# Kernel tuning notes

Measured on AMD Instinct MI355X. Metric: run time of the kernel, lower is better.

The kernel has to match this reference:

```python
import jax, jax.numpy as jnp
import numpy as np

# Pyramid of RBS (Givens) gates on 6 wires: 15 gates, column-major diamond order.
PYRAMID_PAIRS = [(0,1),(1,2),(0,1),(2,3),(1,2),(3,4),(0,1),(2,3),(4,5),(1,2),(3,4),(0,1),(2,3),(1,2),(0,1)]


def setup_inputs() -> dict:
    key = jax.random.key(0)
    k1, k2, k3, k4, k5, k6 = jax.random.split(key, 6)
    B = 65536
    return {
        "inputs": jax.random.normal(k1, (B, 28, 28), dtype=jnp.float32),
        "dense_w": jax.random.normal(k2, (784, 6), dtype=jnp.float32) * 0.05,
        "dense_b": jax.random.normal(k3, (6,), dtype=jnp.float32) * 0.05,
        # module initializes quantum_weights to zeros; use small random angles for a
        # non-degenerate reference (zeros makes the pyramid the identity)
        "qweights": jax.random.normal(k4, (15,), dtype=jnp.float32) * 0.1,
        "out_w": jax.random.normal(k5, (6, 1), dtype=jnp.float32) * 0.5,
        "out_b": jax.random.normal(k6, (1,), dtype=jnp.float32) * 0.1,
    }


def _quantum_block(h, qweights):
    # vector_loader: encode normalized h into unary amplitudes (Hamming-weight-1 subspace)
    a = h / jnp.linalg.norm(h, axis=1, keepdims=True)  # [B, 6]; NaN if zero norm, sanitized below
    # pyramid_circuit: each RBS(theta) acts as a 2x2 Givens rotation on unary amplitudes
    for k, (i, j) in enumerate(PYRAMID_PAIRS):
        c, s = jnp.cos(qweights[k]), jnp.sin(qweights[k])
        ai, aj = a[:, i], a[:, j]
        a = a.at[:, i].set(c * ai + s * aj)
        a = a.at[:, j].set(-s * ai + c * aj)
    # <Z_i> on a unary state = 1 - 2 * P(qubit i = 1) = 1 - 2 * a_i^2
    z = 1.0 - 2.0 * a * a
    return jnp.where(jnp.isnan(z), jnp.zeros_like(z), z)


def reference(inputs, dense_w, dense_b, qweights, out_w, out_b):
    x = inputs.reshape(inputs.shape[0], -1)          # flatten [B, 784]
    h = x @ dense_w + dense_b                        # Dense(6, linear)
    z = _quantum_block(h, qweights)                  # batched statevector sim, [B, 6]
    return jax.nn.sigmoid(z @ out_w + out_b)         # Dense(1, sigmoid)
```

## Files before the change

kernel.cpp:

```cpp
#include <hip/hip_runtime.h>
#include <math.h>

#define TPB 256

__global__ __launch_bounds__(TPB) void hybrid_kernel(
    const float* __restrict__ inp,
    const float* __restrict__ dw,
    const float* __restrict__ db,
    const float* __restrict__ qw,
    const float* __restrict__ ow,
    const float* __restrict__ ob,
    float* __restrict__ out,
    int B)
{
    __shared__ float4 wT4[6 * 196];
    __shared__ float csc[15], css[15];
    __shared__ float sb[8], sw[8];
    __shared__ float sob;

    float* wT = (float*)wT4;
    const int tid = threadIdx.x;

    for (int i = tid; i < 4704; i += TPB) {
        int e = i / 6;
        int j = i - e * 6;
        wT[j * 784 + e] = dw[i];
    }
    if (tid < 15) { float q = qw[tid]; csc[tid] = cosf(q); css[tid] = sinf(q); }
    if (tid < 6)  { sb[tid] = db[tid]; sw[tid] = ow[tid]; }
    if (tid == 0) sob = ob[0];
    __syncthreads();

    const int lane = tid & 63;
    const int grp  = lane >> 4;
    const int gl   = lane & 15;
    const int row  = blockIdx.x * 16 + (tid >> 6) * 4 + grp;
    if (row >= B) return;

    const float4* x4 = (const float4*)(inp + (size_t)row * 784);

    float acc[6] = {0.f, 0.f, 0.f, 0.f, 0.f, 0.f};

    #pragma unroll 4
    for (int t = 0; t < 12; ++t) {
        const int idx4 = gl + 16 * t;
        const float4 xv = x4[idx4];
        #pragma unroll
        for (int j = 0; j < 6; ++j) {
            const float4 wv = wT4[j * 196 + idx4];
            acc[j] += xv.x * wv.x + xv.y * wv.y + xv.z * wv.z + xv.w * wv.w;
        }
    }
    if (gl < 4) {
        const int idx4 = 192 + gl;
        const float4 xv = x4[idx4];
        #pragma unroll
        for (int j = 0; j < 6; ++j) {
            const float4 wv = wT4[j * 196 + idx4];
            acc[j] += xv.x * wv.x + xv.y * wv.y + xv.z * wv.z + xv.w * wv.w;
        }
    }

    #pragma unroll
    for (int m = 1; m <= 8; m <<= 1) {
        #pragma unroll
        for (int j = 0; j < 6; ++j)
            acc[j] += __shfl_xor(acc[j], m, 64);
    }

    float a[6];
    float hh = 0.f;
    #pragma unroll
    for (int j = 0; j < 6; ++j) {
        a[j] = acc[j] + sb[j];
        hh += a[j] * a[j];
    }
    const float inv = rsqrtf(hh);
    #pragma unroll
    for (int j = 0; j < 6; ++j) a[j] *= inv;

    const int PI[15] = {0,1,0,2,1,3,0,2,4,1,3,0,2,1,0};
    #pragma unroll
    for (int k = 0; k < 15; ++k) {
        const int i = PI[k];
        const float c = csc[k], s = css[k];
        const float ai = a[i], aj = a[i + 1];
        a[i]     = c * ai + s * aj;
        a[i + 1] = c * aj - s * ai;
    }

    float v = sob;
    #pragma unroll
    for (int j = 0; j < 6; ++j) {
        float z = 1.f - 2.f * a[j] * a[j];
        z = isnan(z) ? 0.f : z;
        v += z * sw[j];
    }
    const float o = 1.f / (1.f + __expf(-v));

    if (gl == 0) out[row] = o;
}

extern "C" void kernel_launch(void* const* d_in, const int* in_sizes, int n_in,
                              void* d_out, int out_size, void* d_ws, size_t ws_size,
                              hipStream_t stream) {
    const float* inp = (const float*)d_in[0];
    const float* dw  = (const float*)d_in[1];
    const float* db  = (const float*)d_in[2];
    const float* qw  = (const float*)d_in[3];
    const float* ow  = (const float*)d_in[4];
    const float* ob  = (const float*)d_in[5];
    float* out = (float*)d_out;

    const int B = in_sizes[0] / 784;
    const int blocks = (B + 15) / 16;
    hybrid_kernel<<<blocks, TPB, 0, stream>>>(inp, dw, db, qw, ow, ob, out, B);
}
```

Before: 292.8 us.

## Map one row per thread with register double-buffered input loads

Switches from 16 lanes cooperating per row to one thread per row, streaming the row through two register buffers of float4 chunks so the next chunk's load overlaps the current chunk's dot products. Drops the shared-memory weight transpose and reads the dense weights directly as wave-uniform loads, and computes the rotation sin/cos per thread with fast intrinsics. The cost is uncoalesced strided row accesses across lanes, high register use and far fewer waves in flight.

```diff
diff --git a/kernel.cpp b/kernel.cpp
--- a/kernel.cpp
+++ b/kernel.cpp
@@ -1,9 +1,27 @@
 #include <hip/hip_runtime.h>
 #include <math.h>
 
-#define TPB 256
+#define TPB 64
+#define CH  14
+#define NC  14
 
-__global__ __launch_bounds__(TPB) void hybrid_kernel(
+
+#define LOAD_CHUNK(BUF, CBASE)                                   \
+    _Pragma("unroll")                                            \
+    for (int i = 0; i < CH; ++i) BUF[i] = x4[(CBASE) * CH + i];
+
+#define COMP_CHUNK(BUF, CBASE)                                   \
+    _Pragma("unroll")                                            \
+    for (int i = 0; i < CH; ++i) {                               \
+        const float* wp = dw + (size_t)(((CBASE) * CH + i) * 24);\
+        const float4 xv = BUF[i];                                \
+        _Pragma("unroll")                                        \
+        for (int j = 0; j < 6; ++j)                              \
+            acc[j] += xv.x * wp[j]      + xv.y * wp[6 + j]       \
+                    + xv.z * wp[12 + j] + xv.w * wp[18 + j];     \
+    }
+
+__global__ __launch_bounds__(TPB, 1) void hybrid_kernel(
     const float* __restrict__ inp,
     const float* __restrict__ dw,
     const float* __restrict__ db,
@@ -13,66 +31,28 @@
     float* __restrict__ out,
     int B)
 {
-    __shared__ float4 wT4[6 * 196];
-    __shared__ float csc[15], css[15];
-    __shared__ float sb[8], sw[8];
-    __shared__ float sob;
-
-    float* wT = (float*)wT4;
-    const int tid = threadIdx.x;
-
-    for (int i = tid; i < 4704; i += TPB) {
-        int e = i / 6;
-        int j = i - e * 6;
-        wT[j * 784 + e] = dw[i];
-    }
-    if (tid < 15) { float q = qw[tid]; csc[tid] = cosf(q); css[tid] = sinf(q); }
-    if (tid < 6)  { sb[tid] = db[tid]; sw[tid] = ow[tid]; }
-    if (tid == 0) sob = ob[0];
-    __syncthreads();
-
-    const int lane = tid & 63;
-    const int grp  = lane >> 4;
-    const int gl   = lane & 15;
-    const int row  = blockIdx.x * 16 + (tid >> 6) * 4 + grp;
+    const int row = blockIdx.x * TPB + threadIdx.x;
     if (row >= B) return;
 
     const float4* x4 = (const float4*)(inp + (size_t)row * 784);
 
     float acc[6] = {0.f, 0.f, 0.f, 0.f, 0.f, 0.f};
+    float4 bufA[CH], bufB[CH];
 
-    #pragma unroll 4
-    for (int t = 0; t < 12; ++t) {
-        const int idx4 = gl + 16 * t;
-        const float4 xv = x4[idx4];
-        #pragma unroll
-        for (int j = 0; j < 6; ++j) {
-            const float4 wv = wT4[j * 196 + idx4];
-            acc[j] += xv.x * wv.x + xv.y * wv.y + xv.z * wv.z + xv.w * wv.w;
-        }
-    }
-    if (gl < 4) {
-        const int idx4 = 192 + gl;
-        const float4 xv = x4[idx4];
-        #pragma unroll
-        for (int j = 0; j < 6; ++j) {
-            const float4 wv = wT4[j * 196 + idx4];
-            acc[j] += xv.x * wv.x + xv.y * wv.y + xv.z * wv.z + xv.w * wv.w;
-        }
-    }
+    LOAD_CHUNK(bufA, 0)
 
     #pragma unroll
-    for (int m = 1; m <= 8; m <<= 1) {
-        #pragma unroll
-        for (int j = 0; j < 6; ++j)
-            acc[j] += __shfl_xor(acc[j], m, 64);
+    for (int c = 1; c < NC; ++c) {
+        if (c & 1) { LOAD_CHUNK(bufB, c) COMP_CHUNK(bufA, c - 1) }
+        else       { LOAD_CHUNK(bufA, c) COMP_CHUNK(bufB, c - 1) }
     }
+    COMP_CHUNK(bufB, NC - 1)
 
     float a[6];
     float hh = 0.f;
     #pragma unroll
     for (int j = 0; j < 6; ++j) {
-        a[j] = acc[j] + sb[j];
+        a[j] = acc[j] + db[j];
         hh += a[j] * a[j];
     }
     const float inv = rsqrtf(hh);
@@ -83,22 +63,21 @@
     #pragma unroll
     for (int k = 0; k < 15; ++k) {
         const int i = PI[k];
-        const float c = csc[k], s = css[k];
+        const float q = qw[k];
+        const float c = __cosf(q), s = __sinf(q);
         const float ai = a[i], aj = a[i + 1];
         a[i]     = c * ai + s * aj;
         a[i + 1] = c * aj - s * ai;
     }
 
-    float v = sob;
+    float v = ob[0];
     #pragma unroll
     for (int j = 0; j < 6; ++j) {
         float z = 1.f - 2.f * a[j] * a[j];
         z = isnan(z) ? 0.f : z;
-        v += z * sw[j];
+        v += z * ow[j];
     }
-    const float o = 1.f / (1.f + __expf(-v));
-
-    if (gl == 0) out[row] = o;
+    out[row] = 1.f / (1.f + __expf(-v));
 }
 
 extern "C" void kernel_launch(void* const* d_in, const int* in_sizes, int n_in,
@@ -113,6 +92,6 @@
     float* out = (float*)d_out;
 
     const int B = in_sizes[0] / 784;
-    const int blocks = (B + 15) / 16;
+    const int blocks = (B + TPB - 1) / TPB;
     hybrid_kernel<<<blocks, TPB, 0, stream>>>(inp, dw, db, qw, ow, ob, out, B);
 }
```

Result: no change. 297.7 us (+1.6%).
